# Kernel tuning notes

Measured on AMD Instinct MI355X. Metric: run time of the kernel, lower is better.

The kernel has to match this reference:

```python
import jax, jax.numpy as jnp
import numpy as np

# Hyperparameters from __init__ defaults / chosen init kwargs
GAMMA_NEG = 4.0
GAMMA_POS = 1.0
CLIP = 0.05
EPS = 1e-8
ALPHA1 = 2.0
ALPHA_OTHER = 0.5
TOP_K = 10

B, C = 2048, 9605


def setup_inputs() -> dict:
    key = jax.random.key(0)
    k_x, k_y, k_c, k_r, k_d, k_o = jax.random.split(key, 6)
    x = jax.random.normal(k_x, (B, C), dtype=jnp.float32)
    y = (jax.random.uniform(k_y, (B, C)) < 0.01).astype(jnp.float32)
    compost_idx = jax.random.randint(k_c, (30,), 0, C, dtype=jnp.int32)
    recycle_idx = jax.random.randint(k_r, (70,), 0, C, dtype=jnp.int32)
    donate_idx = jax.random.randint(k_d, (70,), 0, C, dtype=jnp.int32)
    other_idx = jax.random.randint(k_o, (40,), 0, C, dtype=jnp.int32)
    # dense whitelist mapping: 0 = not in W_human mapping; priority compost>recycle>donate
    wl_map = jnp.zeros((C,), dtype=jnp.int32)
    wl_map = wl_map.at[other_idx].set(4)
    wl_map = wl_map.at[donate_idx].set(3)
    wl_map = wl_map.at[recycle_idx].set(2)
    wl_map = wl_map.at[compost_idx].set(1)
    return {"x": x, "y": y, "compost_idx": compost_idx,
            "recycle_idx": recycle_idx, "donate_idx": donate_idx,
            "wl_map": wl_map}


def reference(x, y, compost_idx, recycle_idx, donate_idx, wl_map):
    b, c = x.shape
    xs_pos = jax.nn.sigmoid(x)
    xs_neg = jnp.minimum(1.0 - xs_pos + CLIP, 1.0)  # clip shift, clamp max=1
    # base asymmetric BCE term: y*log(p) + (1-y)*log(1-p+clip)
    base = (y * jnp.log(jnp.maximum(xs_pos, EPS))
            + (1.0 - y) * jnp.log(jnp.maximum(xs_neg, EPS)))  # [B, C]

    # per-sample ground-truth whitelist groups (find_gt_whitelist)
    has1 = jnp.sum(y[:, compost_idx], axis=1) > 0  # [B]
    has2 = jnp.sum(y[:, recycle_idx], axis=1) > 0
    has3 = jnp.sum(y[:, donate_idx], axis=1) > 0
    gt_only4 = ~(has1 | has2 | has3)  # gt_whitelist == [4]

    # top-10 predicted classes (argsort descending, first 10)
    _, top_idx = jax.lax.top_k(xs_pos, TOP_K)  # [B, 10]
    rows = jnp.arange(b)

    def step(carry, j):
        # j: [B] class index at current rank; sequential over rank (order matters)
        mult, found = carry
        wl = wl_map[j]                      # group id of this class, 0 if unmapped
        in_map = wl > 0
        in_gt = (((wl == 1) & has1) | ((wl == 2) & has2)
                 | ((wl == 3) & has3) | ((wl == 4) & gt_only4))
        f = jnp.where(in_map & gt_only4, ALPHA_OTHER, 1.0)
        f = f * jnp.where(in_map & (~in_gt) & (~found), ALPHA1, 1.0)
        mult = mult.at[rows, j].multiply(f)
        found = found | (in_map & in_gt)
        return (mult, found), None

    init = (jnp.ones((b, c), x.dtype), jnp.zeros((b,), dtype=bool))
    (mult, found), _ = jax.lax.scan(step, init, top_idx.T)  # scan over 10 ranks

    # if no gt-whitelist match found in top-10: multiply all top-10 by alpha1 again
    extra = jnp.where(found[:, None], 1.0, ALPHA1)  # [B, 1]
    mult = mult.at[rows[:, None], top_idx].multiply(
        jnp.broadcast_to(extra, (b, TOP_K)))

    # asymmetric focal weighting (computed without grad in original)
    pt = xs_pos * y + xs_neg * (1.0 - y)
    gamma = GAMMA_POS * y + GAMMA_NEG * (1.0 - y)
    w = jax.lax.stop_gradient(jnp.power(1.0 - pt, gamma))

    return -jnp.sum(base * mult * w)
```

## Files before the change

kernel.cpp:

```cpp
#include <hip/hip_runtime.h>

#define TOPK 10
#define CLIP 0.05f
#define EPSV 1e-8f
#define ALPHA1 2.0f
#define ALPHA_OTHER 0.5f
#define TCAND 2.5f
#define MAXC 256
#define LN2F 0.69314718056f

__device__ __forceinline__ unsigned long long pack_vc(float v, int c, int C) {
  unsigned u = __float_as_uint(v);
  unsigned key = (u & 0x80000000u) ? ~u : (u | 0x80000000u);
  return ((unsigned long long)key << 32) | (unsigned)(C - c);
}
__device__ __forceinline__ float unpack_v(unsigned long long p) {
  unsigned key = (unsigned)(p >> 32);
  unsigned u = (key & 0x80000000u) ? (key & 0x7fffffffu) : ~key;
  return __uint_as_float(u);
}
__device__ __forceinline__ int unpack_c(unsigned long long p, int C) {
  return C - (int)(unsigned)(p & 0xffffffffu);
}

__device__ __forceinline__ float base_w(float xv, bool pos) {
  float u = __expf(-xv);
  float r = __builtin_amdgcn_rcpf(1.f + u);
  float xneg = fminf(1.05f - r, 1.f);
  float q = pos ? r : xneg;
  float b2 = __log2f(fmaxf(q, EPSV));
  float t = 1.f - q;
  float t2 = t * t;
  float w = pos ? t : t2 * t2;
  return b2 * w;
}


__global__ __launch_bounds__(256) void asl_kernel(
    const float* __restrict__ x, const float* __restrict__ y,
    const int* __restrict__ compost, const int* __restrict__ recycle,
    const int* __restrict__ donate, const int* __restrict__ wl_map,
    float* __restrict__ out, int C, int n1, int n2, int n3)
{
  const int row = blockIdx.x;
  const float* xr = x + (size_t)row * (size_t)C;
  const float* yr = y + (size_t)row * (size_t)C;
  const int tid = threadIdx.x;
  const int lane = tid & 63;
  const int wave = tid >> 6;

  __shared__ float s_x[2][1024];
  __shared__ float s_y[2][1024];
  __shared__ int s_has[3];
  __shared__ unsigned s_cnt;
  __shared__ unsigned long long s_cand[MAXC];
  __shared__ float s_sum[4];
  __shared__ unsigned long long s_top[TOPK];

  if (tid < 3) s_has[tid] = 0;
  if (tid == 0) s_cnt = 0;
  __syncthreads();

  const int ntot = n1 + n2 + n3;
  float gflag = 0.f; int gwhich = -1;
  if (tid < ntot) {
    int colI;
    if (tid < n1)           { gwhich = 0; colI = compost[tid]; }
    else if (tid < n1 + n2) { gwhich = 1; colI = recycle[tid - n1]; }
    else                    { gwhich = 2; colI = donate[tid - n1 - n2]; }
    gflag = yr[colI];
  }

  float ssc = 0.f;

#define PUSH(V, CCOL)                                                     \
  do {                                                                    \
    unsigned _i = atomicAdd(&s_cnt, 1u);                                  \
    if (_i < MAXC) s_cand[_i] = pack_vc((V), (CCOL), C);                  \
  } while (0)
#define PROC_DIRECT(XV, YV, COL)                                          \
  do {                                                                    \
    float _xv = (XV);                                                     \
    ssc += base_w(_xv, (YV) > 0.5f);                                      \
    if (_xv > TCAND) PUSH(_xv, (COL));                                    \
  } while (0)

  int lead = (int)((4u - ((unsigned)((size_t)row * (size_t)C) & 3u)) & 3u);
  if (lead > C) lead = C;
  for (int col = tid; col < lead; col += 256) PROC_DIRECT(xr[col], yr[col], col);

  const int nvec  = (C - lead) >> 2;
  const int nvec4 = nvec << 2;
  const float4* __restrict__ x4 = (const float4*)(xr + lead);
  const float4* __restrict__ y4 = (const float4*)(yr + lead);
  const int ntiles = (nvec + 255) >> 8;

  const unsigned wl4 = (unsigned)(wave * 64 + lane);
  const int wbase = wave * 256;

#define STAGE(T, B)                                                          \
  do {                                                                       \
    unsigned _g4 = (unsigned)(T) * 256u + wl4;                               \
    if (_g4 >= (unsigned)nvec) _g4 = (unsigned)nvec - 1u;     \
    __builtin_amdgcn_global_load_lds(                                        \
        (__attribute__((address_space(1))) void*)(void*)(x4 + _g4),          \
        (__attribute__((address_space(3))) void*)(&s_x[(B)][wbase]),         \
        16, 0, 0);                                                           \
    __builtin_amdgcn_global_load_lds(                                        \
        (__attribute__((address_space(1))) void*)(void*)(y4 + _g4),          \
        (__attribute__((address_space(3))) void*)(&s_y[(B)][wbase]),         \
        16, 0, 0);                                                           \
  } while (0)

  float acc[4] = {0.f, 0.f, 0.f, 0.f};

  if (ntiles > 0) {
    STAGE(0, 0);
    int buf = 0;
    for (int t = 0; t < ntiles; ++t) {
      if (t + 1 < ntiles) {
        STAGE(t + 1, buf ^ 1);
        asm volatile("s_waitcnt vmcnt(2)" ::: "memory");
      } else {
        asm volatile("s_waitcnt vmcnt(0)" ::: "memory");
      }
      const int tb = t * 1024 + wbase;
#pragma unroll
      for (int k = 0; k < 4; ++k) {
        const int off  = k * 64 + lane;
        const int fidx = tb + off;
        if (fidx < nvec4) {
          float xv = s_x[buf][wbase + off];
          float yv = s_y[buf][wbase + off];
          acc[k] += base_w(xv, yv > 0.5f);
          if (xv > TCAND) PUSH(xv, lead + fidx);
        }
      }
      buf ^= 1;
    }
  }

  for (int col = lead + nvec4 + tid; col < C; col += 256)
    PROC_DIRECT(xr[col], yr[col], col);

  if (gwhich >= 0 && gflag > 0.5f) s_has[gwhich] = 1;
  for (int i = 256 + tid; i < ntot; i += 256) {
    int which, colI;
    if (i < n1)           { which = 0; colI = compost[i]; }
    else if (i < n1 + n2) { which = 1; colI = recycle[i - n1]; }
    else                  { which = 2; colI = donate[i - n1 - n2]; }
    if (yr[colI] > 0.5f) s_has[which] = 1;
  }
#undef PROC_DIRECT
#undef PUSH
#undef STAGE

  float sum = ssc + acc[0] + acc[1] + acc[2] + acc[3];
#pragma unroll
  for (int off = 32; off > 0; off >>= 1) sum += __shfl_xor(sum, off, 64);
  if (lane == 0) s_sum[wave] = sum;
  __syncthreads();

  if (wave == 0) {
    const unsigned cnt = s_cnt;
    unsigned long long ls[TOPK];
#pragma unroll
    for (int s = 0; s < TOPK; s++) ls[s] = 0ULL;

#define INSERT(P)                                                          \
    do {                                                                   \
      unsigned long long _p = (P);                                         \
      if (_p > ls[TOPK - 1]) {                                             \
        _Pragma("unroll")                                                  \
        for (int _s = 0; _s < TOPK; _s++) {                                \
          bool _g = _p > ls[_s];                                           \
          unsigned long long _t = _g ? ls[_s] : _p;                        \
          ls[_s] = _g ? _p : ls[_s];                                       \
          _p = _t;                                                         \
        }                                                                  \
      }                                                                    \
    } while (0)

    if (cnt >= TOPK && cnt <= MAXC) {
      for (unsigned i = lane; i < cnt; i += 64) INSERT(s_cand[i]);
    } else {
      for (int col = lane; col < C; col += 64) INSERT(pack_vc(xr[col], col, C));
    }
#undef INSERT

    for (int r = 0; r < TOPK; r++) {
      unsigned long long mine = ls[0];
      unsigned long long best = mine;
#pragma unroll
      for (int off = 32; off > 0; off >>= 1) {
        unsigned long long o = __shfl_xor(best, off, 64);
        best = (o > best) ? o : best;
      }
      if (lane == 0) s_top[r] = best;
      if (mine == best) {
#pragma unroll
        for (int s = 0; s < TOPK - 1; s++) ls[s] = ls[s + 1];
        ls[TOPK - 1] = 0ULL;
      }
    }
  }
  __syncthreads();

  if (tid == 0) {
    float total = s_sum[0] + s_sum[1] + s_sum[2] + s_sum[3];
    const bool h1 = s_has[0] != 0, h2 = s_has[1] != 0, h3 = s_has[2] != 0;
    const bool gt4 = !(h1 || h2 || h3);

    bool found = false;
    float fr[TOPK];
#pragma unroll
    for (int r = 0; r < TOPK; r++) {
      int col = unpack_c(s_top[r], C);
      int wl = wl_map[col];
      bool in_map = wl > 0;
      bool in_gt = (wl == 1 && h1) || (wl == 2 && h2) ||
                   (wl == 3 && h3) || (wl == 4 && gt4);
      float f = 1.f;
      if (in_map && gt4) f *= ALPHA_OTHER;
      if (in_map && !in_gt && !found) f *= ALPHA1;
      fr[r] = f;
      found = found || (in_map && in_gt);
    }
    const float extra = found ? 1.f : ALPHA1;
#pragma unroll
    for (int r = 0; r < TOPK; r++) {
      float mult = fr[r] * extra;
      if (mult != 1.f) {
        int col = unpack_c(s_top[r], C);
        float xv = unpack_v(s_top[r]);
        float bwv = base_w(xv, yr[col] > 0.5f);
        total += (mult - 1.f) * bwv;
      }
    }
    atomicAdd(out, -total * LN2F);
  }
}

extern "C" void kernel_launch(void* const* d_in, const int* in_sizes, int n_in,
                              void* d_out, int out_size, void* d_ws, size_t ws_size,
                              hipStream_t stream) {
  const float* x       = (const float*)d_in[0];
  const float* y       = (const float*)d_in[1];
  const int*   compost = (const int*)d_in[2];
  const int*   recycle = (const int*)d_in[3];
  const int*   donate  = (const int*)d_in[4];
  const int*   wl_map  = (const int*)d_in[5];
  float* out = (float*)d_out;

  const int C  = in_sizes[5];
  const int B  = in_sizes[0] / C;
  const int n1 = in_sizes[2], n2 = in_sizes[3], n3 = in_sizes[4];

  hipMemsetAsync(out, 0, sizeof(float), stream);
  asl_kernel<<<B, 256, 0, stream>>>(x, y, compost, recycle, donate, wl_map,
                                    out, C, n1, n2, n3);
}
```

Before: 211.4 us.

## Deepen LDS staging pipeline to four buffers and read tiles as float4

```diff
diff --git a/kernel.cpp b/kernel.cpp
--- a/kernel.cpp
+++ b/kernel.cpp
@@ -49,8 +49,8 @@
   const int lane = tid & 63;
   const int wave = tid >> 6;
 
-  __shared__ float s_x[2][1024];
-  __shared__ float s_y[2][1024];
+  __shared__ float s_x[4][1024];
+  __shared__ float s_y[4][1024];
   __shared__ int s_has[3];
   __shared__ unsigned s_cnt;
   __shared__ unsigned long long s_cand[MAXC];
@@ -112,31 +112,41 @@
         16, 0, 0);                                                           \
   } while (0)
 
-  float acc[4] = {0.f, 0.f, 0.f, 0.f};
+  float4 accv = make_float4(0.f, 0.f, 0.f, 0.f);
 
   if (ntiles > 0) {
-    STAGE(0, 0);
-    int buf = 0;
+    int issued = 0;
+    for (; issued < 4 && issued < ntiles; ++issued) STAGE(issued, issued);
+
     for (int t = 0; t < ntiles; ++t) {
-      if (t + 1 < ntiles) {
-        STAGE(t + 1, buf ^ 1);
-        asm volatile("s_waitcnt vmcnt(2)" ::: "memory");
-      } else {
-        asm volatile("s_waitcnt vmcnt(0)" ::: "memory");
-      }
-      const int tb = t * 1024 + wbase;
-#pragma unroll
-      for (int k = 0; k < 4; ++k) {
-        const int off  = k * 64 + lane;
-        const int fidx = tb + off;
-        if (fidx < nvec4) {
-          float xv = s_x[buf][wbase + off];
-          float yv = s_y[buf][wbase + off];
-          acc[k] += base_w(xv, yv > 0.5f);
-          if (xv > TCAND) PUSH(xv, lead + fidx);
+      const int rem = issued - t - 1;
+      if (rem >= 3)      asm volatile("s_waitcnt vmcnt(6)" ::: "memory");
+      else if (rem == 2) asm volatile("s_waitcnt vmcnt(4)" ::: "memory");
+      else if (rem == 1) asm volatile("s_waitcnt vmcnt(2)" ::: "memory");
+      else               asm volatile("s_waitcnt vmcnt(0)" ::: "memory");
+
+      const int buf = t & 3;
+      const unsigned g4t = (unsigned)t * 256u + wl4;
+      const float4 X = *(const float4*)&s_x[buf][wbase + lane * 4];
+      const float4 Y = *(const float4*)&s_y[buf][wbase + lane * 4];
+
+      if (g4t < (unsigned)nvec) {
+        const int cb = lead + (int)(g4t * 4u);
+        accv.x += base_w(X.x, Y.x > 0.5f);
+        accv.y += base_w(X.y, Y.y > 0.5f);
+        accv.z += base_w(X.z, Y.z > 0.5f);
+        accv.w += base_w(X.w, Y.w > 0.5f);
+        const float mx = fmaxf(fmaxf(X.x, X.y), fmaxf(X.z, X.w));
+        if (mx > TCAND) {
+          if (X.x > TCAND) PUSH(X.x, cb + 0);
+          if (X.y > TCAND) PUSH(X.y, cb + 1);
+          if (X.z > TCAND) PUSH(X.z, cb + 2);
+          if (X.w > TCAND) PUSH(X.w, cb + 3);
         }
       }
-      buf ^= 1;
+
+      asm volatile("s_waitcnt lgkmcnt(0)" ::: "memory");
+      if (issued < ntiles) { STAGE(issued, issued & 3); ++issued; }
     }
   }
 
@@ -155,7 +165,7 @@
 #undef PUSH
 #undef STAGE
 
-  float sum = ssc + acc[0] + acc[1] + acc[2] + acc[3];
+  float sum = ssc + accv.x + accv.y + accv.z + accv.w;
 #pragma unroll
   for (int off = 32; off > 0; off >>= 1) sum += __shfl_xor(sum, off, 64);
   if (lane == 0) s_sum[wave] = sum;
```

New measurement: 207.8 us. No clear change (-1.7%).
